# Optimization experiments

Measured on AMD Instinct MI355X. Metric: run time of the kernel, lower is better.

Reference implementation:

```python
import jax, jax.numpy as jnp
import numpy as np

TEMPERATURE = 0.07


def setup_inputs() -> dict:
    key = jax.random.key(0)
    k1, k2 = jax.random.split(key)
    B, D = 8192, 1024
    emb1 = jax.random.normal(k1, (B, D), dtype=jnp.float32)
    emb2 = jax.random.normal(k2, (B, D), dtype=jnp.float32)
    return {"emb1": emb1, "emb2": emb2}


def reference(emb1, emb2):
    B = emb1.shape[0]
    # [B, B] similarity logits scaled by temperature
    logits = jnp.matmul(emb1, emb2.T) / TEMPERATURE
    # SigLIP-style contrastive loss: diagonal entries are positives,
    # off-diagonal entries are negatives.
    # positive: -logsigmoid(logits) on diag; negative: -logsigmoid(-logits) off-diag
    pos = -jax.nn.log_sigmoid(jnp.diagonal(logits))            # [B]
    neg = -jax.nn.log_sigmoid(-logits)                          # [B, B]
    # negative_mask zeroes the diagonal -> subtract diagonal contribution
    neg_sum = neg.sum() - jnp.sum(jnp.diagonal(neg))
    loss = (pos.sum() + neg_sum) / B
    return loss
```

## Files before the change

### kernel.cpp

```cpp
#include <hip/hip_runtime.h>


#define B_DIM 8192
#define K_DIM 1024
#define BKB 128
#define NT (K_DIM / BKB)
#define BRICK 16384
#define PANEL_BYTES (NT * BRICK)
#define BUFSZ 49152

typedef int i32x4 __attribute__((ext_vector_type(4)));
typedef int i32x8 __attribute__((ext_vector_type(8)));
typedef float f32x4 __attribute__((ext_vector_type(4)));

__device__ __forceinline__ void brick_store(const float* __restrict__ in,
                                            unsigned char* __restrict__ out,
                                            float scale, int i) {
  const int o = i * 16;
  const int b = o >> 14;
  const int p = b >> 3, t = b & 7;
  const int w = o & (BRICK - 1);
  const int fb = w >> 11;
  const int h = (w >> 10) & 1;
  const int kch = (w >> 8) & 3;
  const int lr = (w >> 4) & 15;
  const int row = p * 128 + fb * 16 + lr;
  const int kb = t * 128 + kch * 32 + h * 16;
  const float4* src = (const float4*)(in + (size_t)row * K_DIM + kb);
  float4 v0 = src[0], v1 = src[1], v2 = src[2], v3 = src[3];
  unsigned w0 = 0, w1 = 0, w2 = 0, w3 = 0;
  w0 = __builtin_amdgcn_cvt_pk_fp8_f32(v0.x * scale, v0.y * scale, w0, 0);
  w0 = __builtin_amdgcn_cvt_pk_fp8_f32(v0.z * scale, v0.w * scale, w0, 1);
  w1 = __builtin_amdgcn_cvt_pk_fp8_f32(v1.x * scale, v1.y * scale, w1, 0);
  w1 = __builtin_amdgcn_cvt_pk_fp8_f32(v1.z * scale, v1.w * scale, w1, 1);
  w2 = __builtin_amdgcn_cvt_pk_fp8_f32(v2.x * scale, v2.y * scale, w2, 0);
  w2 = __builtin_amdgcn_cvt_pk_fp8_f32(v2.z * scale, v2.w * scale, w2, 1);
  w3 = __builtin_amdgcn_cvt_pk_fp8_f32(v3.x * scale, v3.y * scale, w3, 0);
  w3 = __builtin_amdgcn_cvt_pk_fp8_f32(v3.z * scale, v3.w * scale, w3, 1);
  *(uint4*)(out + o) = make_uint4(w0, w1, w2, w3);
}

__global__ __launch_bounds__(256) void cvt_fused(
    const float* __restrict__ e1, const float* __restrict__ e2,
    unsigned char* __restrict__ A8, unsigned char* __restrict__ B8,
    int nbA, float scaleA) {
  const int blk = blockIdx.x;
  if (blk < nbA)
    brick_store(e1, A8, scaleA, blk * 256 + threadIdx.x);
  else
    brick_store(e2, B8, 1.0f, (blk - nbA) * 256 + threadIdx.x);
}

template <bool DIAG>
__device__ __forceinline__ float softplus_sum(const f32x4 (&acc)[4][4],
                                              int rbase, int cbase) {
  float lin = 0.f, cor = 0.f;
#pragma unroll
  for (int m = 0; m < 4; ++m) {
#pragma unroll
    for (int n = 0; n < 4; ++n) {
#pragma unroll
      for (int r = 0; r < 4; ++r) {
        float x = acc[m][n][r];
        if (DIAG) {
          int row = rbase + m * 16 + r;
          int col = cbase + n * 16;
          if (row == col) x = -x;
        }
        lin += fmaxf(x, 0.f);
        cor += __logf(1.f + __expf(-fabsf(x)));
      }
    }
  }
  return lin + cor;
}

#define STAGEA(SB, Q, TI)                                                     \
  __builtin_amdgcn_global_load_lds(                                           \
      (const __attribute__((address_space(1))) void*)(const void*)(           \
          srcA + (TI) * BRICK + (Q) * 1024),                                  \
      (__attribute__((address_space(3))) void*)(void*)(                       \
          lds + (SB) + dA + (Q) * 1024),                                      \
      16, 0, 0)
#define STAGEB(SB, Q, TI)                                                     \
  __builtin_amdgcn_global_load_lds(                                           \
      (const __attribute__((address_space(1))) void*)(const void*)(           \
          srcB + (TI) * BRICK + (Q) * 1024),                                  \
      (__attribute__((address_space(3))) void*)(void*)(                       \
          lds + (SB) + dB + (Q) * 1024),                                      \
      16, 0, 0)
#define STAGE6(SB, TI)                                                        \
  STAGEA(SB, 0, TI); STAGEA(SB, 1, TI); STAGEA(SB, 2, TI); STAGEA(SB, 3, TI); \
  STAGEB(SB, 0, TI); STAGEB(SB, 1, TI)

#define LDA(OUT, RB, M)                                                       \
  {                                                                           \
    const unsigned char* _b =                                                 \
        ldsL + ((RB) + ((wr >> 1) * 16384) + (((wr & 1) * 4 + (M)) << 11));   \
    i32x4 _lo = *(const i32x4*)(_b);                                          \
    i32x4 _hi = *(const i32x4*)(_b + 1024);                                   \
    OUT = __builtin_shufflevector(_lo, _hi, 0, 1, 2, 3, 4, 5, 6, 7);          \
  }
#define LDB(OUT, RB, N)                                                       \
  {                                                                           \
    const unsigned char* _b = ldsL + ((RB) + 32768 + ((wc * 4 + (N)) << 11)); \
    i32x4 _lo = *(const i32x4*)(_b);                                          \
    i32x4 _hi = *(const i32x4*)(_b + 1024);                                   \
    OUT = __builtin_shufflevector(_lo, _hi, 0, 1, 2, 3, 4, 5, 6, 7);          \
  }
#define READS(RB, FA, FB)                                                     \
  LDA(FA[0], RB, 0); LDB(FB[0], RB, 0); LDB(FB[1], RB, 1);                    \
  LDB(FB[2], RB, 2); LDB(FB[3], RB, 3);                                       \
  LDA(FA[1], RB, 1); LDA(FA[2], RB, 2); LDA(FA[3], RB, 3)

#define MFMA1(AF, BF, M, N)                                                   \
  acc[M][N] = __builtin_amdgcn_mfma_scale_f32_16x16x128_f8f6f4(               \
      AF, BF, acc[M][N], 0, 0, 0, 127, 0, 127)
#define MFMAS(FA, FB)                                                         \
  __builtin_amdgcn_s_setprio(1);                                              \
  MFMA1(FA[0], FB[0], 0, 0); MFMA1(FA[0], FB[1], 0, 1);                       \
  MFMA1(FA[0], FB[2], 0, 2); MFMA1(FA[0], FB[3], 0, 3);                       \
  MFMA1(FA[1], FB[0], 1, 0); MFMA1(FA[1], FB[1], 1, 1);                       \
  MFMA1(FA[1], FB[2], 1, 2); MFMA1(FA[1], FB[3], 1, 3);                       \
  MFMA1(FA[2], FB[0], 2, 0); MFMA1(FA[2], FB[1], 2, 1);                       \
  MFMA1(FA[2], FB[2], 2, 2); MFMA1(FA[2], FB[3], 2, 3);                       \
  MFMA1(FA[3], FB[0], 3, 0); MFMA1(FA[3], FB[1], 3, 1);                       \
  MFMA1(FA[3], FB[2], 3, 2); MFMA1(FA[3], FB[3], 3, 3);                       \
  __builtin_amdgcn_s_setprio(0)

#define ITER(T, FAc, FBc, FAn, FBn)                                           \
  {                                                                           \
    if ((T) < NT - 2) { STAGE6((((T) + 2) % 3) * BUFSZ, (T) + 2); }           \
    if ((T) < NT - 2) {                                                       \
      asm volatile("s_waitcnt vmcnt(6)" ::: "memory");                        \
    } else if ((T) == NT - 2) {                                               \
      asm volatile("s_waitcnt vmcnt(0)" ::: "memory");                        \
    }                                                                         \
    if ((T) < NT - 1) {                                                       \
      __builtin_amdgcn_s_barrier();                                           \
      __builtin_amdgcn_sched_barrier(0);                                      \
      READS((((T) + 1) % 3) * BUFSZ, FAn, FBn);                               \
    }                                                                         \
    MFMAS(FAc, FBc);                                                          \
  }

__global__ __launch_bounds__(512, 1) void siglip_gemm(
    const unsigned char* __restrict__ A8,
    const unsigned char* __restrict__ B8,
    float* __restrict__ partials) {
  __shared__ unsigned char lds[3 * BUFSZ];
  __shared__ float wsum[8];

  const int tid = threadIdx.x;
  const int wave = tid >> 6;
  const int lane = tid & 63;
  const int wr = wave >> 1;
  const int wc = wave & 1;
  const int brow = blockIdx.y;
  const int bcol = blockIdx.x;

  f32x4 acc[4][4];
#pragma unroll
  for (int m = 0; m < 4; ++m)
#pragma unroll
    for (int n = 0; n < 4; ++n) acc[m][n] = f32x4{0.f, 0.f, 0.f, 0.f};

  const unsigned char* srcA = A8 +
      (size_t)(2 * brow + (wave >> 2)) * PANEL_BYTES + (wave & 3) * 4096 +
      (lane << 4);
  const unsigned char* srcB =
      B8 + (size_t)bcol * PANEL_BYTES + wave * 2048 + (lane << 4);
  const int dA = (wave >> 2) * 16384 + (wave & 3) * 4096;
  const int dB = 32768 + wave * 2048;
  const unsigned char* ldsL = lds + (lane << 4);

  i32x8 fa0[4], fb0[4], fa1[4], fb1[4];

  STAGE6(0, 0);
  STAGE6(BUFSZ, 1);
  asm volatile("s_waitcnt vmcnt(6)" ::: "memory");
  __builtin_amdgcn_s_barrier();
  __builtin_amdgcn_sched_barrier(0);
  READS(0, fa0, fb0);

  ITER(0, fa0, fb0, fa1, fb1)
  ITER(1, fa1, fb1, fa0, fb0)
  ITER(2, fa0, fb0, fa1, fb1)
  ITER(3, fa1, fb1, fa0, fb0)
  ITER(4, fa0, fb0, fa1, fb1)
  ITER(5, fa1, fb1, fa0, fb0)
  ITER(6, fa0, fb0, fa1, fb1)
  ITER(7, fa1, fb1, fa0, fb0)

  const int rbase = brow * 256 + wr * 64 + (lane >> 4) * 4;
  const int cbase = bcol * 128 + wc * 64 + (lane & 15);
  float lsum;
  if ((bcol >> 1) == brow)
    lsum = softplus_sum<true>(acc, rbase, cbase);
  else
    lsum = softplus_sum<false>(acc, rbase, cbase);

#pragma unroll
  for (int off = 32; off > 0; off >>= 1) lsum += __shfl_down(lsum, off);
  __syncthreads();
  if (lane == 0) wsum[wave] = lsum;
  __syncthreads();
  if (tid == 0) {
    float s = 0.f;
#pragma unroll
    for (int w = 0; w < 8; ++w) s += wsum[w];
    partials[blockIdx.y * gridDim.x + blockIdx.x] = s;
  }
}

__global__ void reduce_kernel(const float* __restrict__ partials, int n,
                              float* __restrict__ out) {
  __shared__ float s[256];
  float v = 0.f;
  for (int i = threadIdx.x; i < n; i += 256) v += partials[i];
  s[threadIdx.x] = v;
  __syncthreads();
  for (int off = 128; off > 0; off >>= 1) {
    if ((int)threadIdx.x < off) s[threadIdx.x] += s[threadIdx.x + off];
    __syncthreads();
  }
  if (threadIdx.x == 0) out[0] = s[0] / (float)B_DIM;
}

extern "C" void kernel_launch(void* const* d_in, const int* in_sizes, int n_in,
                              void* d_out, int out_size, void* d_ws, size_t ws_size,
                              hipStream_t stream) {
  const float* emb1 = (const float*)d_in[0];
  const float* emb2 = (const float*)d_in[1];

  unsigned char* A8 = (unsigned char*)d_ws;
  unsigned char* B8 = A8 + (size_t)B_DIM * K_DIM;
  float* partials = (float*)(B8 + (size_t)B_DIM * K_DIM);

  const float INV_T = 1.0f / 0.07f;
  const int nbA = (B_DIM * K_DIM / 16) / 256;
  cvt_fused<<<2 * nbA, 256, 0, stream>>>(emb1, emb2, A8, B8, nbA, INV_T);

  dim3 grid(B_DIM / 128, B_DIM / 256);
  siglip_gemm<<<grid, 512, 0, stream>>>(A8, B8, partials);

  const int nparts = (B_DIM / 256) * (B_DIM / 128);
  reduce_kernel<<<1, 256, 0, stream>>>(partials, nparts, (float*)d_out);
}
```

Before: 120.3 us.

## Enlarge GEMM block tile to 256x256 with double-buffered quarter-step pipeline

Result: no change. 122.0 us (+1.4%).

```diff
diff --git a/kernel.cpp b/kernel.cpp
--- a/kernel.cpp
+++ b/kernel.cpp
@@ -7,7 +7,7 @@
 #define NT (K_DIM / BKB)
 #define BRICK 16384
 #define PANEL_BYTES (NT * BRICK)
-#define BUFSZ 49152
+#define BUFSZ 65536
 
 typedef int i32x4 __attribute__((ext_vector_type(4)));
 typedef int i32x8 __attribute__((ext_vector_type(8)));
@@ -52,11 +52,11 @@
 }
 
 template <bool DIAG>
-__device__ __forceinline__ float softplus_sum(const f32x4 (&acc)[4][4],
+__device__ __forceinline__ float softplus_sum(const f32x4 (&acc)[8][4],
                                               int rbase, int cbase) {
   float lin = 0.f, cor = 0.f;
 #pragma unroll
-  for (int m = 0; m < 4; ++m) {
+  for (int m = 0; m < 8; ++m) {
 #pragma unroll
     for (int n = 0; n < 4; ++n) {
 #pragma unroll
@@ -89,113 +89,140 @@
       (__attribute__((address_space(3))) void*)(void*)(                       \
           lds + (SB) + dB + (Q) * 1024),                                      \
       16, 0, 0)
-#define STAGE6(SB, TI)                                                        \
-  STAGEA(SB, 0, TI); STAGEA(SB, 1, TI); STAGEA(SB, 2, TI); STAGEA(SB, 3, TI); \
-  STAGEB(SB, 0, TI); STAGEB(SB, 1, TI)
-
-#define LDA(OUT, RB, M)                                                       \
+#define STG4A(SB, TI) \
+  STAGEA(SB, 0, TI); STAGEA(SB, 1, TI); STAGEA(SB, 2, TI); STAGEA(SB, 3, TI)
+#define STG4B(SB, TI) \
+  STAGEB(SB, 0, TI); STAGEB(SB, 1, TI); STAGEB(SB, 2, TI); STAGEB(SB, 3, TI)
+
+#define LDAF(OUT, RB, MH, I)                                                  \
   {                                                                           \
     const unsigned char* _b =                                                 \
-        ldsL + ((RB) + ((wr >> 1) * 16384) + (((wr & 1) * 4 + (M)) << 11));   \
+        ldsL + ((RB) + wrbase + (((MH) * 4 + (I)) << 11));                    \
     i32x4 _lo = *(const i32x4*)(_b);                                          \
     i32x4 _hi = *(const i32x4*)(_b + 1024);                                   \
     OUT = __builtin_shufflevector(_lo, _hi, 0, 1, 2, 3, 4, 5, 6, 7);          \
   }
-#define LDB(OUT, RB, N)                                                       \
+#define LDBF(OUT, RB, NH, J)                                                  \
   {                                                                           \
-    const unsigned char* _b = ldsL + ((RB) + 32768 + ((wc * 4 + (N)) << 11)); \
+    const unsigned char* _b =                                                 \
+        ldsL + ((RB) + bcbase + (((NH) * 2 + (J)) << 11));                    \
     i32x4 _lo = *(const i32x4*)(_b);                                          \
     i32x4 _hi = *(const i32x4*)(_b + 1024);                                   \
     OUT = __builtin_shufflevector(_lo, _hi, 0, 1, 2, 3, 4, 5, 6, 7);          \
   }
-#define READS(RB, FA, FB)                                                     \
-  LDA(FA[0], RB, 0); LDB(FB[0], RB, 0); LDB(FB[1], RB, 1);                    \
-  LDB(FB[2], RB, 2); LDB(FB[3], RB, 3);                                       \
-  LDA(FA[1], RB, 1); LDA(FA[2], RB, 2); LDA(FA[3], RB, 3)
 
 #define MFMA1(AF, BF, M, N)                                                   \
   acc[M][N] = __builtin_amdgcn_mfma_scale_f32_16x16x128_f8f6f4(               \
       AF, BF, acc[M][N], 0, 0, 0, 127, 0, 127)
-#define MFMAS(FA, FB)                                                         \
+
+#define BARLG                                                                 \
+  __builtin_amdgcn_s_barrier();                                               \
+  asm volatile("s_waitcnt lgkmcnt(0)" ::: "memory");                          \
+  __builtin_amdgcn_sched_barrier(0)
+
+#define MF8(A0, A1, A2, A3, BB0, BB1, MH, NH)                                 \
   __builtin_amdgcn_s_setprio(1);                                              \
-  MFMA1(FA[0], FB[0], 0, 0); MFMA1(FA[0], FB[1], 0, 1);                       \
-  MFMA1(FA[0], FB[2], 0, 2); MFMA1(FA[0], FB[3], 0, 3);                       \
-  MFMA1(FA[1], FB[0], 1, 0); MFMA1(FA[1], FB[1], 1, 1);                       \
-  MFMA1(FA[1], FB[2], 1, 2); MFMA1(FA[1], FB[3], 1, 3);                       \
-  MFMA1(FA[2], FB[0], 2, 0); MFMA1(FA[2], FB[1], 2, 1);                       \
-  MFMA1(FA[2], FB[2], 2, 2); MFMA1(FA[2], FB[3], 2, 3);                       \
-  MFMA1(FA[3], FB[0], 3, 0); MFMA1(FA[3], FB[1], 3, 1);                       \
-  MFMA1(FA[3], FB[2], 3, 2); MFMA1(FA[3], FB[3], 3, 3);                       \
+  MFMA1(A0, BB0, (MH)*4 + 0, (NH)*2 + 0);                                     \
+  MFMA1(A0, BB1, (MH)*4 + 0, (NH)*2 + 1);                                     \
+  MFMA1(A1, BB0, (MH)*4 + 1, (NH)*2 + 0);                                     \
+  MFMA1(A1, BB1, (MH)*4 + 1, (NH)*2 + 1);                                     \
+  MFMA1(A2, BB0, (MH)*4 + 2, (NH)*2 + 0);                                     \
+  MFMA1(A2, BB1, (MH)*4 + 2, (NH)*2 + 1);                                     \
+  MFMA1(A3, BB0, (MH)*4 + 3, (NH)*2 + 0);                                     \
+  MFMA1(A3, BB1, (MH)*4 + 3, (NH)*2 + 1);                                     \
   __builtin_amdgcn_s_setprio(0)
 
-#define ITER(T, FAc, FBc, FAn, FBn)                                           \
+#define ITER(T)                                                               \
   {                                                                           \
-    if ((T) < NT - 2) { STAGE6((((T) + 2) % 3) * BUFSZ, (T) + 2); }           \
-    if ((T) < NT - 2) {                                                       \
-      asm volatile("s_waitcnt vmcnt(6)" ::: "memory");                        \
-    } else if ((T) == NT - 2) {                                               \
-      asm volatile("s_waitcnt vmcnt(0)" ::: "memory");                        \
-    }                                                                         \
-    if ((T) < NT - 1) {                                                       \
+    const int rb = ((T) & 1) * BUFSZ;                                         \
+    const int sbuf = rb ^ BUFSZ;                                              \
+    i32x8 bf0, bf1;                                                           \
+    {                                                         \
+      i32x8 af0, af1, af2, af3;                                               \
+      LDBF(bf0, rb, 0, 0); LDBF(bf1, rb, 0, 1);                               \
+      LDAF(af0, rb, 0, 0); LDAF(af1, rb, 0, 1);                               \
+      LDAF(af2, rb, 0, 2); LDAF(af3, rb, 0, 3);                               \
+      if ((T) < NT - 1) { STG4A(sbuf, (T) + 1); }                             \
+      BARLG;                                                                  \
+      MF8(af0, af1, af2, af3, bf0, bf1, 0, 0);                                \
+      __builtin_amdgcn_s_barrier();                                           \
+    }                                                                         \
+    {                                                         \
+      i32x8 af0, af1, af2, af3;                                               \
+      LDAF(af0, rb, 1, 0); LDAF(af1, rb, 1, 1);                               \
+      LDAF(af2, rb, 1, 2); LDAF(af3, rb, 1, 3);                               \
+      if ((T) < NT - 1) { STG4B(sbuf, (T) + 1); }                             \
+      BARLG;                                                                  \
+      MF8(af0, af1, af2, af3, bf0, bf1, 1, 0);                                \
+      __builtin_amdgcn_s_barrier();                                           \
+    }                                                                         \
+    {                                                         \
+      i32x8 af0, af1, af2, af3;                                               \
+      LDBF(bf0, rb, 1, 0); LDBF(bf1, rb, 1, 1);                               \
+      LDAF(af0, rb, 0, 0); LDAF(af1, rb, 0, 1);                               \
+      LDAF(af2, rb, 0, 2); LDAF(af3, rb, 0, 3);                               \
+      BARLG;                                                                  \
+      MF8(af0, af1, af2, af3, bf0, bf1, 0, 1);                                \
+      __builtin_amdgcn_s_barrier();                                           \
+    }                                                                         \
+    {                                                         \
+      i32x8 af0, af1, af2, af3;                                               \
+      LDAF(af0, rb, 1, 0); LDAF(af1, rb, 1, 1);                               \
+      LDAF(af2, rb, 1, 2); LDAF(af3, rb, 1, 3);                               \
+      BARLG;                                                                  \
+      MF8(af0, af1, af2, af3, bf0, bf1, 1, 1);                                \
+      if ((T) < NT - 1) {                                                     \
+        asm volatile("s_waitcnt vmcnt(0)" ::: "memory");                      \
+      }                                                                       \
       __builtin_amdgcn_s_barrier();                                           \
       __builtin_amdgcn_sched_barrier(0);                                      \
-      READS((((T) + 1) % 3) * BUFSZ, FAn, FBn);                               \
-    }                                                                         \
-    MFMAS(FAc, FBc);                                                          \
+    }                                                                         \
   }
 
 __global__ __launch_bounds__(512, 1) void siglip_gemm(
     const unsigned char* __restrict__ A8,
     const unsigned char* __restrict__ B8,
     float* __restrict__ partials) {
-  __shared__ unsigned char lds[3 * BUFSZ];
+  __shared__ unsigned char lds[2 * BUFSZ];
   __shared__ float wsum[8];
 
   const int tid = threadIdx.x;
   const int wave = tid >> 6;
   const int lane = tid & 63;
-  const int wr = wave >> 1;
-  const int wc = wave & 1;
+  const int wr = wave >> 2;
+  const int wc = wave & 3;
   const int brow = blockIdx.y;
   const int bcol = blockIdx.x;
 
-  f32x4 acc[4][4];
-#pragma unroll
-  for (int m = 0; m < 4; ++m)
+  f32x4 acc[8][4];
+#pragma unroll
+  for (int m = 0; m < 8; ++m)
 #pragma unroll
     for (int n = 0; n < 4; ++n) acc[m][n] = f32x4{0.f, 0.f, 0.f, 0.f};
 
   const unsigned char* srcA = A8 +
       (size_t)(2 * brow + (wave >> 2)) * PANEL_BYTES + (wave & 3) * 4096 +
       (lane << 4);
-  const unsigned char* srcB =
-      B8 + (size_t)bcol * PANEL_BYTES + wave * 2048 + (lane << 4);
-  const int dA = (wave >> 2) * 16384 + (wave & 3) * 4096;
-  const int dB = 32768 + wave * 2048;
+  const unsigned char* srcB = B8 +
+      (size_t)(2 * bcol + (wave >> 2)) * PANEL_BYTES + (wave & 3) * 4096 +
+      (lane << 4);
+  const int dA = wave * 4096;
+  const int dB = 32768 + wave * 4096;
+  const int wrbase = wr * 16384;
+  const int bcbase = 32768 + (wc >> 1) * 16384 + ((wc & 1) * 4) * 2048;
   const unsigned char* ldsL = lds + (lane << 4);
 
-  i32x8 fa0[4], fb0[4], fa1[4], fb1[4];
-
-  STAGE6(0, 0);
-  STAGE6(BUFSZ, 1);
-  asm volatile("s_waitcnt vmcnt(6)" ::: "memory");
+  STG4A(0, 0); STG4B(0, 0);
+  asm volatile("s_waitcnt vmcnt(0)" ::: "memory");
   __builtin_amdgcn_s_barrier();
   __builtin_amdgcn_sched_barrier(0);
-  READS(0, fa0, fb0);
-
-  ITER(0, fa0, fb0, fa1, fb1)
-  ITER(1, fa1, fb1, fa0, fb0)
-  ITER(2, fa0, fb0, fa1, fb1)
-  ITER(3, fa1, fb1, fa0, fb0)
-  ITER(4, fa0, fb0, fa1, fb1)
-  ITER(5, fa1, fb1, fa0, fb0)
-  ITER(6, fa0, fb0, fa1, fb1)
-  ITER(7, fa1, fb1, fa0, fb0)
-
-  const int rbase = brow * 256 + wr * 64 + (lane >> 4) * 4;
-  const int cbase = bcol * 128 + wc * 64 + (lane & 15);
+
+  ITER(0) ITER(1) ITER(2) ITER(3) ITER(4) ITER(5) ITER(6) ITER(7)
+
+  const int rbase = brow * 256 + wr * 128 + (lane >> 4) * 4;
+  const int cbase = bcol * 256 + wc * 64 + (lane & 15);
   float lsum;
-  if ((bcol >> 1) == brow)
+  if (brow == bcol)
     lsum = softplus_sum<true>(acc, rbase, cbase);
   else
     lsum = softplus_sum<false>(acc, rbase, cbase);
@@ -241,9 +268,9 @@
   const int nbA = (B_DIM * K_DIM / 16) / 256;
   cvt_fused<<<2 * nbA, 256, 0, stream>>>(emb1, emb2, A8, B8, nbA, INV_T);
 
-  dim3 grid(B_DIM / 128, B_DIM / 256);
+  dim3 grid(B_DIM / 256, B_DIM / 256);
   siglip_gemm<<<grid, 512, 0, stream>>>(A8, B8, partials);
 
-  const int nparts = (B_DIM / 256) * (B_DIM / 128);
+  const int nparts = (B_DIM / 256) * (B_DIM / 256);
   reduce_kernel<<<1, 256, 0, stream>>>(partials, nparts, (float*)d_out);
 }
```
